# Kernel optimization log

Measured on AMD Instinct MI355X. Metric: run time of the kernel, lower is better.

Reference implementation:

```python
import jax, jax.numpy as jnp
import numpy as np

B, H, W, C = 2, 64, 64, 256
NH, K = 8, 7  # num_heads, neighborhood kernel size


def setup_inputs() -> dict:
    key = jax.random.key(0)
    ks = jax.random.split(key, 8)
    xav = lambda k, shape: jax.random.normal(k, shape, jnp.float32) * np.sqrt(2.0 / (shape[0] + shape[1])).astype(np.float32)
    return {
        "x": jax.random.normal(ks[0], (B, H, W, C), jnp.float32),
        "norm1_g": jnp.ones((C,), jnp.float32),
        "norm1_b": jnp.zeros((C,), jnp.float32),
        "qkv_w": xav(ks[1], (3 * C, C)),
        "qkv_b": jnp.zeros((3 * C,), jnp.float32),
        "rpb": jax.random.normal(ks[2], (NH, 2 * K - 1, 2 * K - 1), jnp.float32) * 0.02,
        "proj_w": xav(ks[3], (C, C)),
        "proj_b": jnp.zeros((C,), jnp.float32),
        "norm2_g": jnp.ones((C,), jnp.float32),
        "norm2_b": jnp.zeros((C,), jnp.float32),
        "fc1_w": xav(ks[4], (4 * C, C)),
        "fc1_b": jnp.zeros((4 * C,), jnp.float32),
        "fc2_w": xav(ks[5], (C, 4 * C)),
        "fc2_b": jnp.zeros((C,), jnp.float32),
    }


def _layernorm(x, g, b, eps=1e-5):
    m = x.mean(-1, keepdims=True)
    v = jnp.mean((x - m) ** 2, axis=-1, keepdims=True)
    return (x - m) * jax.lax.rsqrt(v + eps) * g + b


def _nat2d(x, qkv_w, qkv_b, rpb, proj_w, proj_b):
    """Neighborhood attention 2D (NATTEN semantics: edge-clamped k x k windows,
    relative positional bias indexed by key_pos - query_pos + k - 1)."""
    b, h, w, c = x.shape
    nh = rpb.shape[0]
    k = (rpb.shape[1] + 1) // 2
    dh = c // nh
    qkv = (x @ qkv_w.T + qkv_b).reshape(b, h, w, 3, nh, dh)
    q = qkv[..., 0, :, :] * (dh ** -0.5)  # [b,h,w,nh,dh]
    kk = qkv[..., 1, :, :]
    vv = qkv[..., 2, :, :]
    # edge-clamped window starts per query row/col
    starts_h = jnp.clip(jnp.arange(h) - k // 2, 0, h - k)
    starts_w = jnp.clip(jnp.arange(w) - k // 2, 0, w - k)
    idx_h = starts_h[:, None] + jnp.arange(k)  # [h,k] key row indices
    idx_w = starts_w[:, None] + jnp.arange(k)  # [w,k] key col indices
    # gather neighborhoods -> [b,h,w,k,k,nh,dh]
    knb = kk[:, idx_h][:, :, :, idx_w].transpose(0, 1, 3, 2, 4, 5, 6)
    vnb = vv[:, idx_h][:, :, :, idx_w].transpose(0, 1, 3, 2, 4, 5, 6)
    attn = jnp.einsum('bijhd,bijklhd->bijhkl', q, knb)  # [b,h,w,nh,k,k]
    # relative positional bias: index = key - query + (k-1) in [0, 2k-2]
    rb_h = idx_h - jnp.arange(h)[:, None] + (k - 1)  # [h,k]
    rb_w = idx_w - jnp.arange(w)[:, None] + (k - 1)  # [w,k]
    bias = rpb[:, rb_h][:, :, :, rb_w]  # [nh,h,k,w,k]
    bias = bias.transpose(1, 3, 0, 2, 4)  # [h,w,nh,k,k]
    attn = jax.nn.softmax((attn + bias).reshape(b, h, w, nh, k * k), axis=-1)
    out = jnp.einsum('bijhn,bijnhd->bijhd', attn, vnb.reshape(b, h, w, k * k, nh, dh))
    return out.reshape(b, h, w, c) @ proj_w.T + proj_b


def reference(x, norm1_g, norm1_b, qkv_w, qkv_b, rpb, proj_w, proj_b,
              norm2_g, norm2_b, fc1_w, fc1_b, fc2_w, fc2_b):
    # norm -> neighborhood attention -> residual
    x = x + _nat2d(_layernorm(x, norm1_g, norm1_b), qkv_w, qkv_b, rpb, proj_w, proj_b)
    # norm -> MLP (gelu) -> residual
    hdn = _layernorm(x, norm2_g, norm2_b)
    hdn = jax.nn.gelu(hdn @ fc1_w.T + fc1_b, approximate=False)
    return x + (hdn @ fc2_w.T + fc2_b)
```

## Files before the change

kernel.cpp:

```cpp
#include <hip/hip_runtime.h>

typedef __attribute__((ext_vector_type(8))) short bf16x8;
typedef __attribute__((ext_vector_type(4))) float f32x4;
typedef unsigned short u16;

__device__ __forceinline__ float bf2f(u16 u) {
    return __builtin_bit_cast(float, ((unsigned int)u) << 16);
}
__device__ __forceinline__ u16 f2bf(float f) {
    unsigned int x = __builtin_bit_cast(unsigned int, f);
    x += 0x7FFFu + ((x >> 16) & 1u);
    return (u16)(x >> 16);
}

typedef const __attribute__((address_space(1))) void* gas_t;
typedef __attribute__((address_space(3))) void* las_t;
__device__ __forceinline__ void load_lds16(const u16* g, u16* l) {
    __builtin_amdgcn_global_load_lds((gas_t)g, (las_t)l, 16, 0, 0);
}

__global__ __launch_bounds__(256) void prep_kernel(
    const float* __restrict__ s0, const float* __restrict__ s1,
    const float* __restrict__ s2, const float* __restrict__ s3,
    u16* __restrict__ dst,
    const float* __restrict__ x, const float* __restrict__ g,
    const float* __restrict__ b, u16* __restrict__ y)
{
    if (blockIdx.x < 768) {
        const int i4 = (blockIdx.x * 256 + threadIdx.x) * 4;
        const float* src;
        int off;
        if      (i4 < 196608) { src = s0; off = i4; }
        else if (i4 < 262144) { src = s1; off = i4 - 196608; }
        else if (i4 < 524288) { src = s2; off = i4 - 262144; }
        else                  { src = s3; off = i4 - 524288; }
        float4 v = *(const float4*)(src + off);
        ushort4 o;
        o.x = f2bf(v.x); o.y = f2bf(v.y); o.z = f2bf(v.z); o.w = f2bf(v.w);
        *(ushort4*)(dst + i4) = o;
        return;
    }
    const int tok  = (blockIdx.x - 768) * 4 + (threadIdx.x >> 6);
    const int lane = threadIdx.x & 63;
    float4 v = *(const float4*)(x + (size_t)tok * 256 + lane * 4);
    float s  = v.x + v.y + v.z + v.w;
    float sq = v.x*v.x + v.y*v.y + v.z*v.z + v.w*v.w;
    #pragma unroll
    for (int off = 32; off; off >>= 1) {
        s  += __shfl_xor(s, off);
        sq += __shfl_xor(sq, off);
    }
    float mean = s * (1.0f / 256.0f);
    float var  = sq * (1.0f / 256.0f) - mean * mean;
    float rs   = rsqrtf(var + 1e-5f);
    float4 gv = *(const float4*)(g + lane * 4);
    float4 bv = *(const float4*)(b + lane * 4);
    ushort4 o;
    o.x = f2bf((v.x - mean) * rs * gv.x + bv.x);
    o.y = f2bf((v.y - mean) * rs * gv.y + bv.y);
    o.z = f2bf((v.z - mean) * rs * gv.z + bv.z);
    o.w = f2bf((v.w - mean) * rs * gv.w + bv.w);
    *(ushort4*)(y + (size_t)tok * 256 + lane * 4) = o;
}

template<int BM, int BN, int N, int K, int EPI>
__global__ __launch_bounds__(256) void gemm(
    const u16* __restrict__ A, const u16* __restrict__ W,
    const float* __restrict__ bias, const float* __restrict__ res,
    void* __restrict__ outv)
{
    constexpr int WMT = BM / 32;
    constexpr int WNT = BN / 32;
    constexpr int AR  = BM / 32;
    constexpr int BR  = BN / 32;

    __shared__ u16 As[BM * 64];
    __shared__ u16 Bs[BN * 64];
    const int tid  = threadIdx.x;
    const int lane = tid & 63;
    const int wave = tid >> 6;
    const int m0   = blockIdx.x * BM;
    const int n0   = blockIdx.y * BN;
    const int wm0  = (wave >> 1) * (BM / 2);
    const int wn0  = (wave & 1) * (BN / 2);

    f32x4 acc[WMT][WNT];
    #pragma unroll
    for (int mt = 0; mt < WMT; ++mt)
        #pragma unroll
        for (int nt = 0; nt < WNT; ++nt)
            acc[mt][nt] = (f32x4){0.f, 0.f, 0.f, 0.f};

    int soffA[AR];
    #pragma unroll
    for (int r = 0; r < AR; ++r) {
        const int s   = r * 256 + tid;
        const int row = s >> 3;
        const int c   = (s & 7) ^ (row & 7);
        soffA[r] = row * K + c * 8;
    }
    int soffB[BR];
    #pragma unroll
    for (int r = 0; r < BR; ++r) {
        const int s   = r * 256 + tid;
        const int row = s >> 3;
        const int c   = (s & 7) ^ (row & 7);
        soffB[r] = row * K + c * 8;
    }
    const int fr = lane & 15;
    const int fc = lane >> 4;

    for (int k0 = 0; k0 < K; k0 += 64) {
        __syncthreads();
        #pragma unroll
        for (int r = 0; r < AR; ++r)
            load_lds16(A + (size_t)m0 * K + k0 + soffA[r], As + (r * 256 + tid) * 8);
        #pragma unroll
        for (int r = 0; r < BR; ++r)
            load_lds16(W + (size_t)n0 * K + k0 + soffB[r], Bs + (r * 256 + tid) * 8);
        __syncthreads();
        #pragma unroll
        for (int ks = 0; ks < 2; ++ks) {
            bf16x8 af[WMT], bw[WNT];
            #pragma unroll
            for (int mt = 0; mt < WMT; ++mt) {
                const int rr   = wm0 + mt * 16 + fr;
                const int phys = (ks * 4 + fc) ^ (rr & 7);
                af[mt] = *(const bf16x8*)(As + rr * 64 + phys * 8);
            }
            #pragma unroll
            for (int nt = 0; nt < WNT; ++nt) {
                const int rr   = wn0 + nt * 16 + fr;
                const int phys = (ks * 4 + fc) ^ (rr & 7);
                bw[nt] = *(const bf16x8*)(Bs + rr * 64 + phys * 8);
            }
            #pragma unroll
            for (int mt = 0; mt < WMT; ++mt)
                #pragma unroll
                for (int nt = 0; nt < WNT; ++nt)
                    acc[mt][nt] = __builtin_amdgcn_mfma_f32_16x16x32_bf16(af[mt], bw[nt], acc[mt][nt], 0, 0, 0);
        }
    }

    const int col = lane & 15;
    const int rb  = (lane >> 4) * 4;
    #pragma unroll
    for (int nt = 0; nt < WNT; ++nt) {
        const int n  = n0 + wn0 + nt * 16 + col;
        const float bv = bias[n];
        #pragma unroll
        for (int mt = 0; mt < WMT; ++mt) {
            #pragma unroll
            for (int r = 0; r < 4; ++r) {
                const int m = m0 + wm0 + mt * 16 + rb + r;
                float v = acc[mt][nt][r] + bv;
                if (EPI == 1) {
                    if (n < 256) v *= 0.1767766952966369f;
                    ((u16*)outv)[(size_t)m * N + n] = f2bf(v);
                }
                if (EPI == 2) {
                    v += res[(size_t)m * N + n];
                    ((float*)outv)[(size_t)m * N + n] = v;
                }
                if (EPI == 3) {
                    v = 0.5f * v * (1.0f + erff(v * 0.7071067811865475f));
                    ((u16*)outv)[(size_t)m * N + n] = f2bf(v);
                }
            }
        }
    }
}

__global__ __launch_bounds__(512) void attn_proj_kernel(
    const u16* __restrict__ qkv, const float* __restrict__ rpb,
    const u16* __restrict__ projW, const float* __restrict__ proj_b,
    const float* __restrict__ xres, const float* __restrict__ g2,
    const float* __restrict__ b2, float* __restrict__ x1,
    u16* __restrict__ ln2)
{
    __shared__ u16   ao[16 * 256];
    __shared__ float rpbs[8 * 177];
    __shared__ float red[8][16][2];

    const int tid = threadIdx.x;
    const int l   = tid & 63;
    const int w   = tid >> 6;
    const int B   = blockIdx.x;
    const int tile = (B & 7) * 64 + (B >> 3);
    const int bb   = tile >> 8;
    const int rem  = tile & 255;
    const int ti0  = (rem >> 4) << 2;
    const int tj0  = (rem & 15) << 2;
    const int oh   = min(max(ti0 - 3, 0), 54);
    const int ow   = min(max(tj0 - 3, 0), 54);
    const int tokbase = bb * 4096;

    #pragma unroll
    for (int r = 0; r < 3; ++r) {
        const int idx = r * 512 + tid;
        if (idx < 1416) {
            const int hh = idx / 177;
            const int ii = idx - hh * 177;
            rpbs[idx] = (ii < 169) ? rpb[hh * 169 + ii] : -1e30f;
        }
    }

    const int q = l & 15;
    const int g = l >> 4;

    const int tokq = tokbase + (ti0 + (q >> 2)) * 64 + (tj0 + (q & 3));
    const bf16x8 qf = *(const bf16x8*)(qkv + (size_t)tokq * 768 + w * 32 + g * 8);
    bf16x8 kf[7];
    #pragma unroll
    for (int t = 0; t < 7; ++t) {
        const int key = 16 * t + q;
        const int kkc = min(key, 99);
        const int tr  = (kkc * 205) >> 11, tc = kkc - tr * 10;
        const int tokg = tokbase + (oh + tr) * 64 + (ow + tc);
        kf[t] = *(const bf16x8*)(qkv + (size_t)tokg * 768 + 256 + w * 32 + g * 8);
    }

    const int i  = ti0 + (q >> 2), j = tj0 + (q & 3);
    const int sh = min(max(i - 3, 0), 57), sw = min(max(j - 3, 0), 57);
    const int khb = sh - oh, kwb = sw - ow;
    const int bh0 = oh - i + 6, bw0 = ow - j + 6;
    int bidx[7][4];
    int vtok[7][4];
    #pragma unroll
    for (int t = 0; t < 7; ++t)
        #pragma unroll
        for (int r = 0; r < 4; ++r) {
            const int kk  = 16 * t + 4 * g + r;
            const int kkc = min(kk, 99);
            const int hr  = (kkc * 205) >> 11;
            const int hc  = kkc - hr * 10;
            vtok[t][r] = tokbase + (oh + hr) * 64 + (ow + hc);
            const bool valid = (kk < 100)
                && ((unsigned)(hr - khb) < 7u) && ((unsigned)(hc - kwb) < 7u);
            bidx[t][r] = valid ? (bh0 + hr) * 13 + (bw0 + hc) : 169;
        }

    __syncthreads();

    f32x4 S[7];
    #pragma unroll
    for (int t = 0; t < 7; ++t)
        S[t] = __builtin_amdgcn_mfma_f32_16x16x32_bf16(kf[t], qf, (f32x4){0.f,0.f,0.f,0.f}, 0, 0, 0);

    const float* rpbh = rpbs + w * 177;
    float p[7][4];
    float mx = -1e30f;
    #pragma unroll
    for (int t = 0; t < 7; ++t)
        #pragma unroll
        for (int r = 0; r < 4; ++r) {
            const float v = S[t][r] + rpbh[bidx[t][r]];
            p[t][r] = v;
            mx = fmaxf(mx, v);
        }
    mx = fmaxf(mx, __shfl_xor(mx, 16));
    mx = fmaxf(mx, __shfl_xor(mx, 32));
    float sum = 0.f;
    #pragma unroll
    for (int t = 0; t < 7; ++t)
        #pragma unroll
        for (int r = 0; r < 4; ++r) {
            const float e = __expf(p[t][r] - mx);
            p[t][r] = e;
            sum += e;
        }
    sum += __shfl_xor(sum, 16);
    sum += __shfl_xor(sum, 32);
    const float inv = 1.f / sum;

    f32x4 O0 = {0.f,0.f,0.f,0.f}, O1 = {0.f,0.f,0.f,0.f};
    const u16* vbase = qkv + 512 + w * 32 + q;
    #pragma unroll
    for (int kt = 0; kt < 4; ++kt) {
        const int t0   = 2 * kt;
        const bool has1 = (2 * kt + 1) < 7;
        const int t1   = has1 ? 2 * kt + 1 : 2 * kt;
        bf16x8 ph, pl, vA, vB;
        #pragma unroll
        for (int jj = 0; jj < 4; ++jj) {
            const float a = p[t0][jj] * inv;
            const u16 ha = f2bf(a);
            ph[jj] = (short)ha;
            pl[jj] = (short)f2bf(a - bf2f(ha));
            const float b = has1 ? p[t1][jj] * inv : 0.f;
            const u16 hb = f2bf(b);
            ph[4 + jj] = (short)hb;
            pl[4 + jj] = (short)f2bf(b - bf2f(hb));
            vA[jj]     = (short)vbase[(size_t)vtok[t0][jj] * 768];
            vB[jj]     = (short)vbase[(size_t)vtok[t0][jj] * 768 + 16];
            vA[4 + jj] = (short)vbase[(size_t)vtok[t1][jj] * 768];
            vB[4 + jj] = (short)vbase[(size_t)vtok[t1][jj] * 768 + 16];
        }
        O0 = __builtin_amdgcn_mfma_f32_16x16x32_bf16(ph, vA, O0, 0, 0, 0);
        O0 = __builtin_amdgcn_mfma_f32_16x16x32_bf16(pl, vA, O0, 0, 0, 0);
        O1 = __builtin_amdgcn_mfma_f32_16x16x32_bf16(ph, vB, O1, 0, 0, 0);
        O1 = __builtin_amdgcn_mfma_f32_16x16x32_bf16(pl, vB, O1, 0, 0, 0);
    }

    #pragma unroll
    for (int r = 0; r < 4; ++r) {
        const int row = g * 4 + r;
        const int c0  = w * 4 + (q >> 3);
        const int c1  = c0 + 2;
        ao[row * 256 + ((c0 ^ (row & 7)) << 3) + (q & 7)] = f2bf(O0[r]);
        ao[row * 256 + ((c1 ^ (row & 7)) << 3) + (q & 7)] = f2bf(O1[r]);
    }
    __syncthreads();

    const int fr  = l & 15;
    const int fc  = l >> 4;
    const int n0w = w * 32;
    f32x4 pacc[2];
    pacc[0] = (f32x4){0.f,0.f,0.f,0.f};
    pacc[1] = (f32x4){0.f,0.f,0.f,0.f};
    #pragma unroll
    for (int ks = 0; ks < 8; ++ks) {
        const int physA = (ks * 4 + fc) ^ (fr & 7);
        const bf16x8 af = *(const bf16x8*)(ao + fr * 256 + physA * 8);
        #pragma unroll
        for (int nt = 0; nt < 2; ++nt) {
            const int n = n0w + nt * 16 + fr;
            const bf16x8 bw = *(const bf16x8*)(projW + (size_t)n * 256 + ks * 32 + fc * 8);
            pacc[nt] = __builtin_amdgcn_mfma_f32_16x16x32_bf16(af, bw, pacc[nt], 0, 0, 0);
        }
    }

    const int col = l & 15;
    const int rb  = (l >> 4) * 4;
    float vv[2][4];
    float s[4]  = {0.f, 0.f, 0.f, 0.f};
    float sq[4] = {0.f, 0.f, 0.f, 0.f};
    #pragma unroll
    for (int nt = 0; nt < 2; ++nt) {
        const int n = n0w + nt * 16 + col;
        const float bv = proj_b[n];
        #pragma unroll
        for (int r = 0; r < 4; ++r) {
            const int t = rb + r;
            const size_t gi = (size_t)(tokbase + (ti0 + (t >> 2)) * 64 + (tj0 + (t & 3))) * 256 + n;
            float v = pacc[nt][r] + bv + xres[gi];
            x1[gi] = v;
            vv[nt][r] = v;
            s[r]  += v;
            sq[r] += v * v;
        }
    }
    #pragma unroll
    for (int off = 1; off < 16; off <<= 1) {
        #pragma unroll
        for (int r = 0; r < 4; ++r) {
            s[r]  += __shfl_xor(s[r], off);
            sq[r] += __shfl_xor(sq[r], off);
        }
    }
    if (col == 0) {
        #pragma unroll
        for (int r = 0; r < 4; ++r) {
            red[w][rb + r][0] = s[r];
            red[w][rb + r][1] = sq[r];
        }
    }
    __syncthreads();
    float mean[4], rsv[4];
    #pragma unroll
    for (int r = 0; r < 4; ++r) {
        float ts = 0.f, tq = 0.f;
        #pragma unroll
        for (int ww = 0; ww < 8; ++ww) {
            ts += red[ww][rb + r][0];
            tq += red[ww][rb + r][1];
        }
        mean[r] = ts * (1.0f / 256.0f);
        const float var = tq * (1.0f / 256.0f) - mean[r] * mean[r];
        rsv[r]  = rsqrtf(var + 1e-5f);
    }
    #pragma unroll
    for (int nt = 0; nt < 2; ++nt) {
        const int n = n0w + nt * 16 + col;
        const float gv  = g2[n];
        const float bv2 = b2[n];
        #pragma unroll
        for (int r = 0; r < 4; ++r) {
            const int t = rb + r;
            const size_t gi = (size_t)(tokbase + (ti0 + (t >> 2)) * 64 + (tj0 + (t & 3))) * 256 + n;
            ln2[gi] = f2bf((vv[nt][r] - mean[r]) * rsv[r] * gv + bv2);
        }
    }
}

extern "C" void kernel_launch(void* const* d_in, const int* in_sizes, int n_in,
                              void* d_out, int out_size, void* d_ws, size_t ws_size,
                              hipStream_t stream)
{
    const float* x      = (const float*)d_in[0];
    const float* n1g    = (const float*)d_in[1];
    const float* n1b    = (const float*)d_in[2];
    const float* qkv_w  = (const float*)d_in[3];
    const float* qkv_b  = (const float*)d_in[4];
    const float* rpb    = (const float*)d_in[5];
    const float* proj_w = (const float*)d_in[6];
    const float* proj_b = (const float*)d_in[7];
    const float* n2g    = (const float*)d_in[8];
    const float* n2b    = (const float*)d_in[9];
    const float* fc1_w  = (const float*)d_in[10];
    const float* fc1_b  = (const float*)d_in[11];
    const float* fc2_w  = (const float*)d_in[12];
    const float* fc2_b  = (const float*)d_in[13];
    float* out = (float*)d_out;

    char* wsb = (char*)d_ws;
    u16*   wbf   = (u16*)wsb;
    u16*   qkvW  = wbf;
    u16*   projW = wbf + 196608;
    u16*   fc1W  = wbf + 262144;
    u16*   fc2W  = wbf + 524288;
    u16*   ln1   = (u16*)(wsb + 1572864);
    u16*   qkvB  = (u16*)(wsb + 5767168);
    u16*   hbuf  = (u16*)(wsb + 9961472);
    float* x1    = (float*)(wsb + 26738688);
    u16*   ln2   = (u16*)(wsb + 35651584);

    dim3 blk(256);
    prep_kernel<<<2816, blk, 0, stream>>>(qkv_w, proj_w, fc1_w, fc2_w, wbf,
                                          x, n1g, n1b, ln1);
    gemm<128, 64, 768, 256, 1><<<dim3(64, 12), blk, 0, stream>>>(ln1, qkvW, qkv_b, nullptr, qkvB);
    attn_proj_kernel<<<512, dim3(512), 0, stream>>>(qkvB, rpb, projW, proj_b, x, n2g, n2b, x1, ln2);
    gemm<128, 64, 1024, 256, 3><<<dim3(64, 16), blk, 0, stream>>>(ln2, fc1W, fc1_b, nullptr, hbuf);
    gemm<128, 64, 256, 1024, 2><<<dim3(64, 4), blk, 0, stream>>>(hbuf, fc2W, fc2_b, x1, out);
}
```

Measured before the change: 147.1 us.

## Load GEMM weight fragments directly from global memory, stage only A in LDS

The templated GEMM is replaced by a variant that stages a 64x256 A tile in LDS with one sync pair per 256-wide K block, and reads B (weight) fragments straight from global memory into registers instead of through LDS. M tile shrinks from 128 to 64, doubling the grid. The aim is fewer barriers and less LDS traffic, plus more blocks for occupancy. The cost is uncoalesced, latency-exposed global loads for weights, relying on cache reuse across blocks, and less per-block reuse of A.

```diff
diff --git a/kernel.cpp b/kernel.cpp
--- a/kernel.cpp
+++ b/kernel.cpp
@@ -63,81 +63,68 @@
     *(ushort4*)(y + (size_t)tok * 256 + lane * 4) = o;
 }
 
-template<int BM, int BN, int N, int K, int EPI>
-__global__ __launch_bounds__(256) void gemm(
+template<int BN, int N, int K, int EPI>
+__global__ __launch_bounds__(256) void gemm_direct(
     const u16* __restrict__ A, const u16* __restrict__ W,
     const float* __restrict__ bias, const float* __restrict__ res,
     void* __restrict__ outv)
 {
-    constexpr int WMT = BM / 32;
-    constexpr int WNT = BN / 32;
-    constexpr int AR  = BM / 32;
-    constexpr int BR  = BN / 32;
-
-    __shared__ u16 As[BM * 64];
-    __shared__ u16 Bs[BN * 64];
+    constexpr int KB = K / 256;
+    __shared__ u16 As[64 * 256];
     const int tid  = threadIdx.x;
     const int lane = tid & 63;
     const int wave = tid >> 6;
-    const int m0   = blockIdx.x * BM;
+    const int m0   = blockIdx.x * 64;
     const int n0   = blockIdx.y * BN;
-    const int wm0  = (wave >> 1) * (BM / 2);
-    const int wn0  = (wave & 1) * (BN / 2);
-
-    f32x4 acc[WMT][WNT];
-    #pragma unroll
-    for (int mt = 0; mt < WMT; ++mt)
-        #pragma unroll
-        for (int nt = 0; nt < WNT; ++nt)
+    const int wm0  = (wave >> 1) * 32;
+    const int wn0  = (wave & 1) * 32;
+
+    f32x4 acc[2][2];
+    #pragma unroll
+    for (int mt = 0; mt < 2; ++mt)
+        #pragma unroll
+        for (int nt = 0; nt < 2; ++nt)
             acc[mt][nt] = (f32x4){0.f, 0.f, 0.f, 0.f};
 
-    int soffA[AR];
-    #pragma unroll
-    for (int r = 0; r < AR; ++r) {
+    int soff[8];
+    #pragma unroll
+    for (int r = 0; r < 8; ++r) {
         const int s   = r * 256 + tid;
-        const int row = s >> 3;
-        const int c   = (s & 7) ^ (row & 7);
-        soffA[r] = row * K + c * 8;
-    }
-    int soffB[BR];
-    #pragma unroll
-    for (int r = 0; r < BR; ++r) {
-        const int s   = r * 256 + tid;
-        const int row = s >> 3;
-        const int c   = (s & 7) ^ (row & 7);
-        soffB[r] = row * K + c * 8;
+        const int row = s >> 5;
+        const int pc  = s & 31;
+        const int gc  = (pc & 24) | ((pc & 7) ^ (row & 7));
+        soff[r] = row * K + gc * 8;
     }
     const int fr = lane & 15;
     const int fc = lane >> 4;
 
-    for (int k0 = 0; k0 < K; k0 += 64) {
+    const u16* Abase = A + (size_t)m0 * K;
+
+    for (int kb = 0; kb < KB; ++kb) {
         __syncthreads();
         #pragma unroll
-        for (int r = 0; r < AR; ++r)
-            load_lds16(A + (size_t)m0 * K + k0 + soffA[r], As + (r * 256 + tid) * 8);
-        #pragma unroll
-        for (int r = 0; r < BR; ++r)
-            load_lds16(W + (size_t)n0 * K + k0 + soffB[r], Bs + (r * 256 + tid) * 8);
+        for (int r = 0; r < 8; ++r)
+            load_lds16(Abase + kb * 256 + soff[r], As + (r * 256 + tid) * 8);
         __syncthreads();
         #pragma unroll
-        for (int ks = 0; ks < 2; ++ks) {
-            bf16x8 af[WMT], bw[WNT];
+        for (int kk = 0; kk < 8; ++kk) {
+            const int ci = kk * 4 + fc;
+            bf16x8 af[2], bw[2];
             #pragma unroll
-            for (int mt = 0; mt < WMT; ++mt) {
+            for (int mt = 0; mt < 2; ++mt) {
                 const int rr   = wm0 + mt * 16 + fr;
-                const int phys = (ks * 4 + fc) ^ (rr & 7);
-                af[mt] = *(const bf16x8*)(As + rr * 64 + phys * 8);
+                const int phys = (ci & 24) | ((ci & 7) ^ (rr & 7));
+                af[mt] = *(const bf16x8*)(As + rr * 256 + phys * 8);
             }
             #pragma unroll
-            for (int nt = 0; nt < WNT; ++nt) {
-                const int rr   = wn0 + nt * 16 + fr;
-                const int phys = (ks * 4 + fc) ^ (rr & 7);
-                bw[nt] = *(const bf16x8*)(Bs + rr * 64 + phys * 8);
+            for (int nt = 0; nt < 2; ++nt) {
+                const int n = n0 + wn0 + nt * 16 + fr;
+                bw[nt] = *(const bf16x8*)(W + (size_t)n * K + kb * 256 + ci * 8);
             }
             #pragma unroll
-            for (int mt = 0; mt < WMT; ++mt)
+            for (int mt = 0; mt < 2; ++mt)
                 #pragma unroll
-                for (int nt = 0; nt < WNT; ++nt)
+                for (int nt = 0; nt < 2; ++nt)
                     acc[mt][nt] = __builtin_amdgcn_mfma_f32_16x16x32_bf16(af[mt], bw[nt], acc[mt][nt], 0, 0, 0);
         }
     }
@@ -145,11 +132,11 @@
     const int col = lane & 15;
     const int rb  = (lane >> 4) * 4;
     #pragma unroll
-    for (int nt = 0; nt < WNT; ++nt) {
+    for (int nt = 0; nt < 2; ++nt) {
         const int n  = n0 + wn0 + nt * 16 + col;
         const float bv = bias[n];
         #pragma unroll
-        for (int mt = 0; mt < WMT; ++mt) {
+        for (int mt = 0; mt < 2; ++mt) {
             #pragma unroll
             for (int r = 0; r < 4; ++r) {
                 const int m = m0 + wm0 + mt * 16 + rb + r;
@@ -428,8 +415,8 @@
     dim3 blk(256);
     prep_kernel<<<2816, blk, 0, stream>>>(qkv_w, proj_w, fc1_w, fc2_w, wbf,
                                           x, n1g, n1b, ln1);
-    gemm<128, 64, 768, 256, 1><<<dim3(64, 12), blk, 0, stream>>>(ln1, qkvW, qkv_b, nullptr, qkvB);
+    gemm_direct<64, 768, 256, 1><<<dim3(128, 12), blk, 0, stream>>>(ln1, qkvW, qkv_b, nullptr, qkvB);
     attn_proj_kernel<<<512, dim3(512), 0, stream>>>(qkvB, rpb, projW, proj_b, x, n2g, n2b, x1, ln2);
-    gemm<128, 64, 1024, 256, 3><<<dim3(64, 16), blk, 0, stream>>>(ln2, fc1W, fc1_b, nullptr, hbuf);
-    gemm<128, 64, 256, 1024, 2><<<dim3(64, 4), blk, 0, stream>>>(hbuf, fc2W, fc2_b, x1, out);
-}
+    gemm_direct<64, 1024, 256, 3><<<dim3(128, 16), blk, 0, stream>>>(ln2, fc1W, fc1_b, nullptr, hbuf);
+    gemm_direct<64, 256, 1024, 2><<<dim3(128, 4), blk, 0, stream>>>(hbuf, fc2W, fc2_b, x1, out);
+}
```

Result: slower. 173.5 us (+17.9%).
